# Kernel optimization log

Hardware: AMD Instinct MI355X
Metric: run time of the kernel (lower is better)

## Reference

```python
import jax, jax.numpy as jnp
import numpy as np


def _segment_mean(msg, dst, num_nodes):
    # msg: [E, B, O, T] summed into [N, B, O, T], mean over incoming edges
    s = jax.ops.segment_sum(msg, dst, num_segments=num_nodes)
    cnt = jax.ops.segment_sum(jnp.ones((msg.shape[0],), msg.dtype), dst, num_segments=num_nodes)
    return s / jnp.clip(cnt, 1.0)[:, None, None, None]


def _gcn(x, edge_index, edge_attr, A, Wk, Wr, b):
    # Edge-conditioned (spline-style) graph conv.
    # x: [B, N, Cin, T]; edge_attr: [E, 3]; Wk: [K, Cin, Cout]
    N = x.shape[1]
    src, dst = edge_index[0], edge_index[1]
    Bw = jax.nn.softmax(edge_attr @ A, axis=-1)          # [E, K] basis weights
    We = jnp.einsum('ek,kio->eio', Bw, Wk)                # [E, Cin, Cout]
    msg = jnp.einsum('beit,eio->ebot', x[:, src], We)     # [E, B, Cout, T]
    agg = _segment_mean(msg, dst, N).transpose(1, 0, 2, 3)  # [B, N, Cout, T]
    out = agg + jnp.einsum('bnit,io->bnot', x, Wr) + b[None, None, :, None]
    return jax.nn.elu(out)


def _pool(x, P, C, T):
    # x: [B, N_l, C, T] -> flatten, sparse-pool with P [N_{l+1}, N_l], unflatten
    B, N = x.shape[0], x.shape[1]
    xf = x.reshape(B, N, C * T)
    xf = jnp.einsum('mn,bnf->bmf', P, xf)
    return xf.reshape(B, P.shape[0], C, T)


def setup_inputs() -> dict:
    key = jax.random.key(0)
    ks = jax.random.split(key, 24)
    B, T = 2, 200
    N = [2048, 512, 128, 64]
    E = [16384, 8192, 2048]
    nf = [1, 8, 16, 32, 64, 128, 128]
    ld = 64

    def rn(k, shape, scale=1.0):
        return jax.random.normal(k, shape, dtype=jnp.float32) * scale

    inp = {}
    inp['x'] = rn(ks[0], (B, N[0], nf[0], T))
    inp['ei0'] = jax.random.randint(ks[1], (2, E[0]), 0, N[0])
    inp['ea0'] = jax.random.uniform(ks[2], (E[0], 3), dtype=jnp.float32)
    inp['ei1'] = jax.random.randint(ks[3], (2, E[1]), 0, N[1])
    inp['ea1'] = jax.random.uniform(ks[4], (E[1], 3), dtype=jnp.float32)
    inp['ei2'] = jax.random.randint(ks[5], (2, E[2]), 0, N[2])
    inp['ea2'] = jax.random.uniform(ks[6], (E[2], 3), dtype=jnp.float32)
    # gcn params: (A basis map, K=3 kernel weights, root weight, bias)
    inp['A1'] = rn(ks[7], (3, 3))
    inp['Wk1'] = rn(ks[8], (3, nf[0], nf[2]), 1.0 / np.sqrt(nf[0]))
    inp['Wr1'] = rn(ks[9], (nf[0], nf[2]), 1.0 / np.sqrt(nf[0]))
    inp['b1'] = jnp.zeros((nf[2],), jnp.float32)
    inp['A2'] = rn(ks[10], (3, 3))
    inp['Wk2'] = rn(ks[11], (3, nf[2], nf[3]), 1.0 / np.sqrt(nf[2]))
    inp['Wr2'] = rn(ks[12], (nf[2], nf[3]), 1.0 / np.sqrt(nf[2]))
    inp['b2'] = jnp.zeros((nf[3],), jnp.float32)
    inp['A3'] = rn(ks[13], (3, 3))
    inp['Wk3'] = rn(ks[14], (3, nf[3], nf[4]), 1.0 / np.sqrt(nf[3]))
    inp['Wr3'] = rn(ks[15], (nf[3], nf[4]), 1.0 / np.sqrt(nf[3]))
    inp['b3'] = jnp.zeros((nf[4],), jnp.float32)
    # sparse pooling projections (dense here)
    inp['P01'] = rn(ks[16], (N[1], N[0]), 1.0 / np.sqrt(N[0]))
    inp['P12'] = rn(ks[17], (N[2], N[1]), 1.0 / np.sqrt(N[1]))
    inp['P23'] = rn(ks[18], (N[3], N[2]), 1.0 / np.sqrt(N[2]))
    # 1x1 conv encoder head
    inp['fce1_w'] = rn(ks[19], (nf[4], nf[6]), 1.0 / np.sqrt(nf[4]))
    inp['fce1_b'] = jnp.zeros((nf[6],), jnp.float32)
    inp['fce2_w'] = rn(ks[20], (nf[6], ld), 1.0 / np.sqrt(nf[6]))
    inp['fce2_b'] = jnp.zeros((ld,), jnp.float32)
    return inp


def reference(x, ei0, ea0, ei1, ea1, ei2, ea2, A1, Wk1, Wr1, b1, A2, Wk2, Wr2, b2,
              A3, Wk3, Wr3, b3, P01, P12, P23, fce1_w, fce1_b, fce2_w, fce2_b):
    T = x.shape[-1]
    # level 0 -> 1
    h = _gcn(x, ei0, ea0, A1, Wk1, Wr1, b1)          # [B, N0, 16, T]
    h = _pool(h, P01, h.shape[2], T)                 # [B, N1, 16, T]
    # level 1 -> 2
    h = _gcn(h, ei1, ea1, A2, Wk2, Wr2, b2)          # [B, N1, 32, T]
    h = _pool(h, P12, h.shape[2], T)                 # [B, N2, 32, T]
    # level 2 -> 3
    h = _gcn(h, ei2, ea2, A3, Wk3, Wr3, b3)          # [B, N2, 64, T]
    h = _pool(h, P23, h.shape[2], T)                 # [B, N3, 64, T]
    # 1x1 conv encoder head (channel-wise linear over node/time grid)
    h = jax.nn.elu(jnp.einsum('bnct,co->bnot', h, fce1_w) + fce1_b[None, None, :, None])
    mu = jnp.tanh(jnp.einsum('bnct,co->bnot', h, fce2_w) + fce2_b[None, None, :, None])
    return mu  # [B, N3, latent_dim, T]
```

## Files before the change

kernel.cpp:

```cpp
#include <hip/hip_runtime.h>
#include <hip/hip_bf16.h>

using bf16 = __hip_bfloat16;
typedef unsigned short ushort_t;
typedef unsigned int uint_t;

constexpr int B = 2, T = 200;
constexpr int N0 = 2048, N1 = 512, N2 = 128, N3 = 64;
constexpr int E0 = 16384, E1 = 8192, E2 = 2048;

typedef __attribute__((ext_vector_type(8))) short bf16x8;
typedef __attribute__((ext_vector_type(4))) float f32x4;

constexpr size_t O_FLAG = 161792;
constexpr size_t O_WC1  = 163840;
constexpr size_t O_BIAS = 164096;
constexpr size_t O_BW0  = 165312;
constexpr size_t O_BW1  = 361920;
constexpr size_t O_BW2  = 460224;
constexpr size_t O_PB1  = 484800;
constexpr size_t O_PB2  = 2581952;
constexpr size_t O_PB3  = 2713024;
constexpr size_t O_WT2  = 2729408;
constexpr size_t O_WT3  = 2733504;
constexpr size_t O_W1H  = 2749888;
constexpr size_t O_W2H  = 2766272;
constexpr size_t O_AA   = 2785280;
constexpr size_t O_BB   = 15892480;

__device__ __forceinline__ float ldx(const void* p, long i, int bf) {
  if (bf) {
    uint_t v = (uint_t)(((const ushort_t*)p)[i]) << 16;
    float f; __builtin_memcpy(&f, &v, 4); return f;
  }
  return ((const float*)p)[i];
}
__device__ __forceinline__ void stf(float* p, float v) { *p = v; }
__device__ __forceinline__ void stf(bf16* p, float v) { *p = __float2bfloat16(v); }
__device__ __forceinline__ ushort_t f2bfu(float v) {
  bf16 h = __float2bfloat16(v); ushort_t u; __builtin_memcpy(&u, &h, 2); return u;
}

struct InPtrs {
  const void* ea0; const void* ea1; const void* ea2;
  const void* P01; const void* P12; const void* P23;
  const void* Wk1; const void* Wr1; const void* Wk2; const void* Wr2;
  const void* Wk3; const void* Wr3; const void* W1h; const void* W2h;
  const void* b1; const void* b2; const void* b3; const void* b1h; const void* b2h;
  const void* A1; const void* A2; const void* A3;
};

__global__ void k_setup0(int* I, const ushort_t* ea) {
  if (blockIdx.x < 158) {
    int i = blockIdx.x * 256 + threadIdx.x;
    I[i] = 0;
  } else if (threadIdx.x == 0) {
    int c = 0;
    for (int i = 0; i < 128; ++i) {
      uint_t v = (uint_t)ea[i] << 16;
      float f; __builtin_memcpy(&f, &v, 4);
      if (f >= 0.f && f <= 1.0f) c++;
    }
    *(int*)((char*)I + O_FLAG) = (c >= 120) ? 1 : 0;
  }
}

__device__ __forceinline__ void bw_one(const void* ea, int bf, const void* A,
                                       float* bw, int e) {
  float a0 = ldx(ea, e*3+0, bf), a1 = ldx(ea, e*3+1, bf), a2 = ldx(ea, e*3+2, bf);
  float l0 = a0*ldx(A,0,bf) + a1*ldx(A,3,bf) + a2*ldx(A,6,bf);
  float l1 = a0*ldx(A,1,bf) + a1*ldx(A,4,bf) + a2*ldx(A,7,bf);
  float l2 = a0*ldx(A,2,bf) + a1*ldx(A,5,bf) + a2*ldx(A,8,bf);
  float m = fmaxf(l0, fmaxf(l1, l2));
  float x0 = expf(l0 - m), x1 = expf(l1 - m), x2 = expf(l2 - m);
  float inv = 1.0f / (x0 + x1 + x2);
  bw[e*3+0] = x0*inv; bw[e*3+1] = x1*inv; bw[e*3+2] = x2*inv;
}

__global__ void k_prep(InPtrs P, char* base) {
  int bf = *(const int*)(base + O_FLAG);
  int bx = blockIdx.x, tid = threadIdx.x;
  float* bw0 = (float*)(base + O_BW0);
  float* bw1 = (float*)(base + O_BW1);
  float* bw2 = (float*)(base + O_BW2);
  if (bx < 64)        { bw_one(P.ea0, bf, P.A1, bw0, bx*256+tid); return; }
  if (bx < 96)        { bw_one(P.ea1, bf, P.A2, bw1, (bx-64)*256+tid); return; }
  if (bx < 104)       { bw_one(P.ea2, bf, P.A3, bw2, (bx-96)*256+tid); return; }
  if (bx < 4200)      { long i = (long)(bx-104)*256+tid;
                        ((ushort_t*)(base+O_PB1))[i] = f2bfu(ldx(P.P01, i, bf)); return; }
  if (bx < 4456)      { int i = (bx-4200)*256+tid;
                        ((ushort_t*)(base+O_PB2))[i] = f2bfu(ldx(P.P12, i, bf)); return; }
  if (bx < 4488)      { int i = (bx-4456)*256+tid;
                        ((ushort_t*)(base+O_PB3))[i] = f2bfu(ldx(P.P23, i, bf)); return; }
  if (bx < 4496)      { int j = (bx-4488)*256+tid; int o = j>>6, c = j&63;
                        float v = (c<48) ? ldx(P.Wk2, c*32+o, bf) : ldx(P.Wr2, (c-48)*32+o, bf);
                        ((ushort_t*)(base+O_WT2))[j] = f2bfu(v); return; }
  if (bx < 4528)      { int j = (bx-4496)*256+tid; int o = j>>7, c = j&127;
                        float v = (c<96) ? ldx(P.Wk3, c*64+o, bf) : ldx(P.Wr3, (c-96)*64+o, bf);
                        ((ushort_t*)(base+O_WT3))[j] = f2bfu(v); return; }
  if (bx < 4560)      { int j = (bx-4528)*256+tid; int o = j>>6, c = j&63;
                        ((ushort_t*)(base+O_W1H))[j] = f2bfu(ldx(P.W1h, c*128+o, bf)); return; }
  if (bx < 4592)      { int j = (bx-4560)*256+tid; int o = j>>7, c = j&127;
                        ((ushort_t*)(base+O_W2H))[j] = f2bfu(ldx(P.W2h, c*64+o, bf)); return; }
  {
    int i = (bx-4592)*256+tid;
    if (i < 64) {
      ((float*)(base+O_WC1))[i] = (i<48) ? ldx(P.Wk1, i, bf) : ldx(P.Wr1, i-48, bf);
    } else if (i < 368) {
      int j = i - 64; float v;
      if (j < 16)       v = ldx(P.b1, j, bf);
      else if (j < 48)  v = ldx(P.b2, j-16, bf);
      else if (j < 112) v = ldx(P.b3, j-48, bf);
      else if (j < 240) v = ldx(P.b1h, j-112, bf);
      else              v = ldx(P.b2h, j-240, bf);
      ((float*)(base+O_BIAS))[j] = v;
    }
  }
}

__global__ void k_hist3(const int* d0, const int* d1, const int* d2,
                        int* c0, int* c1, int* c2) {
  int i = blockIdx.x * 256 + threadIdx.x;
  if (i < E0) atomicAdd(&c0[d0[i]], 1);
  if (i < E1) atomicAdd(&c1[d1[i]], 1);
  if (i < E2) atomicAdd(&c2[d2[i]], 1);
}

__global__ void k_scan3(const int* c0, int* o0, int* u0,
                        const int* c1, int* o1, int* u1,
                        const int* c2, int* o2, int* u2) {
  const int* cnt; int* off; int* cur; int N;
  if (blockIdx.x == 0)      { cnt = c0; off = o0; cur = u0; N = N0; }
  else if (blockIdx.x == 1) { cnt = c1; off = o1; cur = u1; N = N1; }
  else                      { cnt = c2; off = o2; cur = u2; N = N2; }
  int tid = threadIdx.x;
  int chunk = (N + 63) >> 6;
  int base = tid * chunk;
  int s = 0;
  for (int j = 0; j < chunk; ++j) { int idx = base + j; if (idx < N) s += cnt[idx]; }
  int pre = s;
  for (int d = 1; d < 64; d <<= 1) {
    int v = __shfl_up(pre, d, 64);
    if (tid >= d) pre += v;
  }
  int run = pre - s;
  for (int j = 0; j < chunk; ++j) {
    int idx = base + j;
    if (idx < N) { off[idx] = run; cur[idx] = run; run += cnt[idx]; }
  }
  if (tid == 63) off[N] = run;
}

__global__ void k_fill3(const int* d0, int* u0, int* e0l,
                        const int* d1, int* u1, int* e1l,
                        const int* d2, int* u2, int* e2l) {
  int i = blockIdx.x * 256 + threadIdx.x;
  if (i < E0) { int p = atomicAdd(&u0[d0[i]], 1); e0l[p] = i; }
  if (i < E1) { int p = atomicAdd(&u1[d1[i]], 1); e1l[p] = i; }
  if (i < E2) { int p = atomicAdd(&u2[d2[i]], 1); e2l[p] = i; }
}

__global__ __launch_bounds__(256) void k_gc1(const void* x, const int* src,
    const int* off, const int* elist, const int* cnt, const float* bw,
    const float* W, const float* bias, bf16* h1, const int* flagp) {
  __shared__ float Wl[64];
  __shared__ float bl[16];
  __shared__ float ew0[32], ew1[32], ew2[32];
  __shared__ int es[32];
  int tid = threadIdx.x;
  if (tid < 64) Wl[tid] = W[tid];
  if (tid < 16) bl[tid] = bias[tid];
  int bf = *flagp;
  int n = blockIdx.y, b = blockIdx.z;
  int t = tid;
  bool tok = t < T;
  int beg = off[n], end = off[n + 1];
  float a0 = 0.f, a1 = 0.f, a2 = 0.f;
  for (int q0 = beg; q0 < end; q0 += 32) {
    int m = end - q0; if (m > 32) m = 32;
    __syncthreads();
    if (tid < m) {
      int e = elist[q0 + tid];
      es[tid] = src[e];
      ew0[tid] = bw[e*3+0]; ew1[tid] = bw[e*3+1]; ew2[tid] = bw[e*3+2];
    }
    __syncthreads();
    if (tok) {
      for (int j = 0; j < m; ++j) {
        float xv = ldx(x, (long)(b * N0 + es[j]) * T + t, bf);
        a0 += ew0[j] * xv; a1 += ew1[j] * xv; a2 += ew2[j] * xv;
      }
    }
  }
  __syncthreads();
  if (!tok) return;
  int c = cnt[n];
  float inv = 1.f / (float)(c > 0 ? c : 1);
  a0 *= inv; a1 *= inv; a2 *= inv;
  float xr = ldx(x, (long)(b * N0 + n) * T + t, bf);
  bf16* op = h1 + ((long)(b * N0 + n) * 16) * T + t;
#pragma unroll
  for (int o = 0; o < 16; ++o) {
    float v = a0 * Wl[o] + a1 * Wl[16 + o] + a2 * Wl[32 + o] + xr * Wl[48 + o] + bl[o];
    v = v > 0.f ? v : (expf(v) - 1.f);
    op[o * T] = __float2bfloat16(v);
  }
}

template<int CIN, int CPI, int O>
__global__ __launch_bounds__(256) void k_gcm(const float* hp, const int* src,
    const int* off, const int* elist, const int* cnt, const float* bw,
    const ushort_t* Wt, const float* bias, bf16* h, int N) {
  constexpr int C = 4 * CIN;
  constexpr int KG = C / 8;
  constexpr int MT = O / 16;
  __shared__ __align__(16) ushort_t Ws[O * C];
  __shared__ __align__(16) ushort_t Is[64 * C];
  __shared__ float ew0[32], ew1[32], ew2[32];
  __shared__ int es[32];
  int tid = threadIdx.x;
  int w = tid >> 6, l = tid & 63;
  int lf = l & 15, quad = l >> 4;
  int t0 = blockIdx.x * 64;
  int n = blockIdx.y, b = blockIdx.z;
  {
    const uint4* Wg = (const uint4*)Wt;
    for (int s = tid; s < O * KG; s += 256) {
      int o = s / KG, kg = s % KG;
      *(uint4*)(Ws + o * C + ((kg ^ (o & 7)) * 8)) = Wg[s];
    }
  }
  int tx = tid & 63, iy = tid >> 6;
  int t = t0 + tx;
  bool tok = t < T;
  float acc[3][CPI], xr[CPI];
#pragma unroll
  for (int k = 0; k < 3; ++k)
#pragma unroll
    for (int j = 0; j < CPI; ++j) acc[k][j] = 0.f;
#pragma unroll
  for (int j = 0; j < CPI; ++j) xr[j] = 0.f;
  int beg = off[n], end = off[n + 1];
  for (int q0 = beg; q0 < end; q0 += 32) {
    int mE = end - q0; if (mE > 32) mE = 32;
    __syncthreads();
    if (tid < mE) {
      int e = elist[q0 + tid];
      es[tid] = src[e];
      ew0[tid] = bw[e*3+0]; ew1[tid] = bw[e*3+1]; ew2[tid] = bw[e*3+2];
    }
    __syncthreads();
    if (tok) {
      for (int j2 = 0; j2 < mE; ++j2) {
        int s = es[j2];
        float w0 = ew0[j2], w1 = ew1[j2], w2 = ew2[j2];
        const float* xp = hp + ((long)(b * N + s) * CIN) * T + t;
#pragma unroll
        for (int j = 0; j < CPI; ++j) {
          float xv = xp[(iy * CPI + j) * T];
          acc[0][j] += w0 * xv; acc[1][j] += w1 * xv; acc[2][j] += w2 * xv;
        }
      }
    }
  }
  float inv = 1.f;
  if (tok) {
    int c = cnt[n];
    inv = 1.f / (float)(c > 0 ? c : 1);
    const float* xs = hp + ((long)(b * N + n) * CIN) * T + t;
#pragma unroll
    for (int j = 0; j < CPI; ++j) xr[j] = xs[(iy * CPI + j) * T];
  }
#pragma unroll
  for (int j = 0; j < CPI; ++j) {
    int i = iy * CPI + j;
#pragma unroll
    for (int k = 0; k < 3; ++k) {
      int c = k * CIN + i;
      Is[tx * C + ((c >> 3) ^ (tx & 7)) * 8 + (c & 7)] = f2bfu(acc[k][j] * inv);
    }
    int c = 3 * CIN + i;
    Is[tx * C + ((c >> 3) ^ (tx & 7)) * 8 + (c & 7)] = f2bfu(xr[j]);
  }
  __syncthreads();
  f32x4 dacc[MT];
#pragma unroll
  for (int mt = 0; mt < MT; ++mt) dacc[mt] = (f32x4){0.f, 0.f, 0.f, 0.f};
  int tr = w * 16 + lf;
#pragma unroll
  for (int kc = 0; kc < C / 32; ++kc) {
    int kg0 = kc * 4 + quad;
    bf16x8 bfr = *(const bf16x8*)(Is + tr * C + ((kg0 ^ (tr & 7)) * 8));
#pragma unroll
    for (int mt = 0; mt < MT; ++mt) {
      int o = mt * 16 + lf;
      bf16x8 afr = *(const bf16x8*)(Ws + o * C + ((kg0 ^ (o & 7)) * 8));
      dacc[mt] = __builtin_amdgcn_mfma_f32_16x16x32_bf16(afr, bfr, dacc[mt], 0, 0, 0);
    }
  }
  int tg = t0 + w * 16 + lf;
  if (tg < T) {
    long nb = (long)(b * N + n) * O;
#pragma unroll
    for (int mt = 0; mt < MT; ++mt) {
#pragma unroll
      for (int r = 0; r < 4; ++r) {
        int o = mt * 16 + quad * 4 + r;
        float v = dacc[mt][r] + bias[o];
        v = v > 0.f ? v : (expf(v) - 1.f);
        h[(nb + o) * T + tg] = __float2bfloat16(v);
      }
    }
  }
}

template<int KSPLIT, bool ATOMIC, bool SWZ>
__global__ __launch_bounds__(256) void k_poolp(const ushort_t* Pb, const ushort_t* h,
                                               float* out, int M, int K, int F, int nInner) {
  __shared__ __align__(16) ushort_t As[64 * 64];
  __shared__ __align__(16) ushort_t Bs[64 * 64];
  int tid = threadIdx.x;
  int w = tid >> 6, l = tid & 63;
  int lf = l & 15, quad = l >> 4;
  int v = blockIdx.x;
  if (SWZ) { int q = gridDim.x >> 3; v = (v & 7) * q + (v >> 3); }
  int f_blk = v / nInner; int rem = v % nInner;
  int m_blk = rem / (KSPLIT * B);
  int kc = (rem / B) % KSPLIT;
  int b = rem % B;
  int f0 = f_blk * 64, m0 = m_blk * 64;
  int Kc = K / KSPLIT;
  int k0 = kc * Kc;
  int nsteps = Kc >> 6;

  int am0 = tid >> 3, ak = tid & 7;
  int am1 = am0 + 32;
  const ushort_t* Ap0 = Pb + (long)(m0 + am0) * K + k0 + ak * 8;
  const ushort_t* Ap1 = Pb + (long)(m0 + am1) * K + k0 + ak * 8;
  int fB = tid & 63, kb = (tid >> 6) * 16;
  const ushort_t* Bp = h + ((long)b * K + k0 + kb) * F + f0 + fB;
  int kc0 = kb >> 3;

#define PLA(r0, r1, st) { r0 = *(const uint4*)(Ap0 + (st) * 64); \
                          r1 = *(const uint4*)(Ap1 + (st) * 64); }
#define PLB(rb, st) { _Pragma("unroll") \
                      for (int i = 0; i < 16; ++i) rb[i] = Bp[(long)((st) * 64 + i) * F]; }
#define PSA(r0, r1) { *(uint4*)(As + am0 * 64 + ((ak ^ (am0 & 7)) * 8)) = r0; \
                      *(uint4*)(As + am1 * 64 + ((ak ^ (am1 & 7)) * 8)) = r1; }
#define PSB(rb) { *(uint4*)(Bs + fB * 64 + ((kc0 ^ (fB & 7)) * 8)) = *(uint4*)&rb[0]; \
                  *(uint4*)(Bs + fB * 64 + (((kc0 + 1) ^ (fB & 7)) * 8)) = *(uint4*)&rb[8]; }
#define PMM() { _Pragma("unroll") for (int ks = 0; ks < 2; ++ks) { \
    int kq = ks * 4 + quad; \
    bf16x8 bfr[4]; \
    _Pragma("unroll") for (int ft = 0; ft < 4; ++ft) { int fl = ft * 16 + lf; \
      bfr[ft] = *(const bf16x8*)(Bs + fl * 64 + ((kq ^ (fl & 7)) * 8)); } \
    int ml = w * 16 + lf; \
    bf16x8 afr = *(const bf16x8*)(As + ml * 64 + ((kq ^ (ml & 7)) * 8)); \
    _Pragma("unroll") for (int ft = 0; ft < 4; ++ft) \
      acc[ft] = __builtin_amdgcn_mfma_f32_16x16x32_bf16(afr, bfr[ft], acc[ft], 0, 0, 0); } }

  f32x4 acc[4];
#pragma unroll
  for (int ft = 0; ft < 4; ++ft) acc[ft] = (f32x4){0.f, 0.f, 0.f, 0.f};

  uint4 ra0, ra1, sa0, sa1;
  ushort_t rb[16], sb[16];
  PLA(ra0, ra1, 0); PLB(rb, 0);
  for (int s = 0; s < nsteps; s += 2) {
    PLA(sa0, sa1, s + 1); PLB(sb, s + 1);
    __syncthreads();
    PSA(ra0, ra1); PSB(rb);
    __syncthreads();
    PMM();
    if (s + 2 < nsteps) { PLA(ra0, ra1, s + 2); PLB(rb, s + 2); }
    __syncthreads();
    PSA(sa0, sa1); PSB(sb);
    __syncthreads();
    PMM();
  }
#undef PLA
#undef PLB
#undef PSA
#undef PSB
#undef PMM

#pragma unroll
  for (int r = 0; r < 4; ++r) {
    int m = m0 + w * 16 + quad * 4 + r;
    float* op = out + ((long)(b * M + m)) * F + f0 + lf;
#pragma unroll
    for (int ft = 0; ft < 4; ++ft) {
      if (ATOMIC) atomicAdd(op + ft * 16, acc[ft][r]);
      else        op[ft * 16] = acc[ft][r];
    }
  }
}

__global__ __launch_bounds__(256) void k_head(const float* hp3, const ushort_t* W1t,
    const ushort_t* W2t, const float* bias, void* outp, const int* flagp) {
  __shared__ __align__(16) ushort_t Ws1[128 * 64];
  __shared__ __align__(16) ushort_t Ws2[64 * 128];
  __shared__ __align__(16) ushort_t Is[64 * 64];
  __shared__ __align__(16) ushort_t G[64 * 128];
  int tid = threadIdx.x;
  int w = tid >> 6, l = tid & 63;
  int lf = l & 15, quad = l >> 4;
  int t0 = blockIdx.x * 64;
  int n = blockIdx.y, b = blockIdx.z;
  {
    const uint4* g1 = (const uint4*)W1t;
    for (int s = tid; s < 1024; s += 256) {
      int o = s >> 3, kg = s & 7;
      *(uint4*)(Ws1 + o * 64 + ((kg ^ (o & 7)) * 8)) = g1[s];
    }
    const uint4* g2 = (const uint4*)W2t;
    for (int s = tid; s < 1024; s += 256) {
      int o = s >> 4, kg = s & 15;
      *(uint4*)(Ws2 + o * 128 + ((kg ^ (o & 7)) * 8)) = g2[s];
    }
  }
  {
    int t = tid & 63;
    bool tok = (t0 + t) < T;
    const float* ip = hp3 + ((long)(b * 64 + n) * 64) * T + t0;
    for (int kg = tid >> 6; kg < 8; kg += 4) {
      ushort_t r[8];
#pragma unroll
      for (int j = 0; j < 8; ++j)
        r[j] = tok ? f2bfu(ip[(kg * 8 + j) * T + t]) : (ushort_t)0;
      *(uint4*)(Is + t * 64 + ((kg ^ (t & 7)) * 8)) = *(uint4*)r;
    }
  }
  __syncthreads();
  int tr = w * 16 + lf;
  {
    f32x4 a1[8];
#pragma unroll
    for (int mt = 0; mt < 8; ++mt) a1[mt] = (f32x4){0.f, 0.f, 0.f, 0.f};
#pragma unroll
    for (int kc = 0; kc < 2; ++kc) {
      int kg0 = kc * 4 + quad;
      bf16x8 bfr = *(const bf16x8*)(Is + tr * 64 + ((kg0 ^ (tr & 7)) * 8));
#pragma unroll
      for (int mt = 0; mt < 8; ++mt) {
        int o = mt * 16 + lf;
        bf16x8 afr = *(const bf16x8*)(Ws1 + o * 64 + ((kg0 ^ (o & 7)) * 8));
        a1[mt] = __builtin_amdgcn_mfma_f32_16x16x32_bf16(afr, bfr, a1[mt], 0, 0, 0);
      }
    }
    int tG = w * 16 + lf;
#pragma unroll
    for (int mt = 0; mt < 8; ++mt) {
#pragma unroll
      for (int r = 0; r < 4; ++r) {
        int o1 = mt * 16 + quad * 4 + r;
        float v = a1[mt][r] + bias[112 + o1];
        v = v > 0.f ? v : (expf(v) - 1.f);
        G[tG * 128 + ((o1 >> 3) ^ (tG & 7)) * 8 + (o1 & 7)] = f2bfu(v);
      }
    }
  }
  __syncthreads();
  {
    f32x4 a2[4];
#pragma unroll
    for (int mt = 0; mt < 4; ++mt) a2[mt] = (f32x4){0.f, 0.f, 0.f, 0.f};
#pragma unroll
    for (int kc = 0; kc < 4; ++kc) {
      int kg0 = kc * 4 + quad;
      bf16x8 bfr = *(const bf16x8*)(G + tr * 128 + ((kg0 ^ (tr & 7)) * 8));
#pragma unroll
      for (int mt = 0; mt < 4; ++mt) {
        int o = mt * 16 + lf;
        bf16x8 afr = *(const bf16x8*)(Ws2 + o * 128 + ((kg0 ^ (o & 7)) * 8));
        a2[mt] = __builtin_amdgcn_mfma_f32_16x16x32_bf16(afr, bfr, a2[mt], 0, 0, 0);
      }
    }
    int t = t0 + w * 16 + lf;
    if (t < T) {
      int bf = *flagp;
      long nb = (long)(b * 64 + n) * 64;
#pragma unroll
      for (int mt = 0; mt < 4; ++mt) {
#pragma unroll
        for (int r = 0; r < 4; ++r) {
          int o2 = mt * 16 + quad * 4 + r;
          float v = tanhf(a2[mt][r] + bias[240 + o2]);
          long idx = (nb + o2) * T + t;
          if (bf) ((bf16*)outp)[idx] = __float2bfloat16(v);
          else    ((float*)outp)[idx] = v;
        }
      }
    }
  }
}

extern "C" void kernel_launch(void* const* d_in, const int* in_sizes, int n_in,
                              void* d_out, int out_size, void* d_ws, size_t ws_size,
                              hipStream_t stream) {
  const int* ei0 = (const int*)d_in[1];
  const int* ei1 = (const int*)d_in[3];
  const int* ei2 = (const int*)d_in[5];

  char* base = (char*)d_ws;
  int* I = (int*)base;
  int* cnt0 = I;         int* off0 = I + 2048;  int* cur0 = I + 4112;  int* el0 = I + 6160;
  int* cnt1 = I + 22544; int* off1 = I + 23056; int* cur1 = I + 23584; int* el1 = I + 24096;
  int* cnt2 = I + 32288; int* off2 = I + 32416; int* cur2 = I + 32560; int* el2 = I + 32688;
  const int* flagp = (const int*)(base + O_FLAG);
  float* wc1f = (float*)(base + O_WC1);
  float* bias = (float*)(base + O_BIAS);
  float* bw0 = (float*)(base + O_BW0);
  float* bw1 = (float*)(base + O_BW1);
  float* bw2 = (float*)(base + O_BW2);
  ushort_t* Pb1 = (ushort_t*)(base + O_PB1);
  ushort_t* Pb2 = (ushort_t*)(base + O_PB2);
  ushort_t* Pb3 = (ushort_t*)(base + O_PB3);
  ushort_t* wt2 = (ushort_t*)(base + O_WT2);
  ushort_t* wt3 = (ushort_t*)(base + O_WT3);
  ushort_t* w1t = (ushort_t*)(base + O_W1H);
  ushort_t* w2t = (ushort_t*)(base + O_W2H);
  char* Aa = base + O_AA;
  char* Bb = base + O_BB;

  InPtrs P = { d_in[2], d_in[4], d_in[6], d_in[19], d_in[20], d_in[21],
               d_in[8], d_in[9], d_in[12], d_in[13], d_in[16], d_in[17],
               d_in[22], d_in[24], d_in[10], d_in[14], d_in[18], d_in[23],
               d_in[25], d_in[7], d_in[11], d_in[15] };

  k_setup0<<<159, 256, 0, stream>>>(I, (const ushort_t*)d_in[2]);
  k_prep<<<4594, 256, 0, stream>>>(P, base);
  k_hist3<<<64, 256, 0, stream>>>(ei0 + E0, ei1 + E1, ei2 + E2, cnt0, cnt1, cnt2);
  k_scan3<<<3, 64, 0, stream>>>(cnt0, off0, cur0, cnt1, off1, cur1, cnt2, off2, cur2);
  k_fill3<<<64, 256, 0, stream>>>(ei0 + E0, cur0, el0, ei1 + E1, cur1, el1, ei2 + E2, cur2, el2);

  hipMemsetAsync(Aa, 0, (size_t)13107200, stream);
  k_gc1<<<dim3(1, N0, B), 256, 0, stream>>>(d_in[0], ei0, off0, el0, cnt0, bw0, wc1f, bias, (bf16*)Bb, flagp);
  k_poolp<2, true, true><<<1600, 256, 0, stream>>>(Pb1, (const ushort_t*)Bb, (float*)Aa, 512, 2048, 3200, 32);
  k_gcm<16, 4, 32><<<dim3(4, N1, B), 256, 0, stream>>>((const float*)Aa, ei1, off1, el1, cnt1, bw1, wt2, bias + 16, (bf16*)Bb, N1);
  hipMemsetAsync(Aa, 0, (size_t)6553600, stream);
  k_poolp<2, true, true><<<800, 256, 0, stream>>>(Pb2, (const ushort_t*)Bb, (float*)Aa, 128, 512, 6400, 8);
  k_gcm<32, 8, 64><<<dim3(4, N2, B), 256, 0, stream>>>((const float*)Aa, ei2, off2, el2, cnt2, bw2, wt3, bias + 48, (bf16*)Bb, N2);
  k_poolp<1, false, false><<<400, 256, 0, stream>>>(Pb3, (const ushort_t*)Bb, (float*)Aa, 64, 128, 12800, 2);
  k_head<<<dim3(4, N3, B), 256, 0, stream>>>((const float*)Aa, w1t, w2t, bias, d_out, flagp);
}
```

Before: 302.4 us.

## Double-buffer pool GEMM LDS tiles and drop split-K atomics with memsets

Rewrites the pooling GEMM kernel to use two LDS buffers per operand, so the MFMA work on one tile overlaps the shared-memory stores of the next. This halves the barriers per step and replaces __syncthreads with a lighter waitcnt plus barrier. It also removes the split-K decomposition, along with its float atomics and the two memsets that zeroed the output. In exchange each block does twice the K work and the grid has half as many blocks, which lowers parallelism on the large pooling stages.

```diff
diff --git a/kernel.cpp b/kernel.cpp
--- a/kernel.cpp
+++ b/kernel.cpp
@@ -314,85 +314,86 @@
   }
 }
 
-template<int KSPLIT, bool ATOMIC, bool SWZ>
+template<bool SWZ>
 __global__ __launch_bounds__(256) void k_poolp(const ushort_t* Pb, const ushort_t* h,
                                                float* out, int M, int K, int F, int nInner) {
-  __shared__ __align__(16) ushort_t As[64 * 64];
-  __shared__ __align__(16) ushort_t Bs[64 * 64];
+  __shared__ __align__(16) ushort_t As0[64 * 64];
+  __shared__ __align__(16) ushort_t As1[64 * 64];
+  __shared__ __align__(16) ushort_t Bs0[64 * 64];
+  __shared__ __align__(16) ushort_t Bs1[64 * 64];
   int tid = threadIdx.x;
   int w = tid >> 6, l = tid & 63;
   int lf = l & 15, quad = l >> 4;
   int v = blockIdx.x;
   if (SWZ) { int q = gridDim.x >> 3; v = (v & 7) * q + (v >> 3); }
   int f_blk = v / nInner; int rem = v % nInner;
-  int m_blk = rem / (KSPLIT * B);
-  int kc = (rem / B) % KSPLIT;
-  int b = rem % B;
+  int m_blk = rem >> 1;
+  int b = rem & 1;
   int f0 = f_blk * 64, m0 = m_blk * 64;
-  int Kc = K / KSPLIT;
-  int k0 = kc * Kc;
-  int nsteps = Kc >> 6;
+  int nsteps = K >> 6;
 
   int am0 = tid >> 3, ak = tid & 7;
   int am1 = am0 + 32;
-  const ushort_t* Ap0 = Pb + (long)(m0 + am0) * K + k0 + ak * 8;
-  const ushort_t* Ap1 = Pb + (long)(m0 + am1) * K + k0 + ak * 8;
+  const ushort_t* Ap0 = Pb + (long)(m0 + am0) * K + ak * 8;
+  const ushort_t* Ap1 = Pb + (long)(m0 + am1) * K + ak * 8;
   int fB = tid & 63, kb = (tid >> 6) * 16;
-  const ushort_t* Bp = h + ((long)b * K + k0 + kb) * F + f0 + fB;
+  const ushort_t* Bp = h + ((long)b * K + kb) * F + f0 + fB;
   int kc0 = kb >> 3;
 
-#define PLA(r0, r1, st) { r0 = *(const uint4*)(Ap0 + (st) * 64); \
-                          r1 = *(const uint4*)(Ap1 + (st) * 64); }
+#define PLA(r0, r1, st) { r0 = *(const uint4*)(Ap0 + (long)(st) * 64); \
+                          r1 = *(const uint4*)(Ap1 + (long)(st) * 64); }
 #define PLB(rb, st) { _Pragma("unroll") \
-                      for (int i = 0; i < 16; ++i) rb[i] = Bp[(long)((st) * 64 + i) * F]; }
-#define PSA(r0, r1) { *(uint4*)(As + am0 * 64 + ((ak ^ (am0 & 7)) * 8)) = r0; \
-                      *(uint4*)(As + am1 * 64 + ((ak ^ (am1 & 7)) * 8)) = r1; }
-#define PSB(rb) { *(uint4*)(Bs + fB * 64 + ((kc0 ^ (fB & 7)) * 8)) = *(uint4*)&rb[0]; \
-                  *(uint4*)(Bs + fB * 64 + (((kc0 + 1) ^ (fB & 7)) * 8)) = *(uint4*)&rb[8]; }
-#define PMM() { _Pragma("unroll") for (int ks = 0; ks < 2; ++ks) { \
+                      for (int i = 0; i < 16; ++i) rb[i] = Bp[((long)(st) * 64 + i) * F]; }
+#define PSA(S, r0, r1) { *(uint4*)(S + am0 * 64 + ((ak ^ (am0 & 7)) * 8)) = r0; \
+                         *(uint4*)(S + am1 * 64 + ((ak ^ (am1 & 7)) * 8)) = r1; }
+#define PSB(S, rb) { *(uint4*)(S + fB * 64 + ((kc0 ^ (fB & 7)) * 8)) = *(uint4*)&rb[0]; \
+                     *(uint4*)(S + fB * 64 + (((kc0 + 1) ^ (fB & 7)) * 8)) = *(uint4*)&rb[8]; }
+#define PMM(SA, SB) { _Pragma("unroll") for (int ks = 0; ks < 2; ++ks) { \
     int kq = ks * 4 + quad; \
     bf16x8 bfr[4]; \
     _Pragma("unroll") for (int ft = 0; ft < 4; ++ft) { int fl = ft * 16 + lf; \
-      bfr[ft] = *(const bf16x8*)(Bs + fl * 64 + ((kq ^ (fl & 7)) * 8)); } \
+      bfr[ft] = *(const bf16x8*)(SB + fl * 64 + ((kq ^ (fl & 7)) * 8)); } \
     int ml = w * 16 + lf; \
-    bf16x8 afr = *(const bf16x8*)(As + ml * 64 + ((kq ^ (ml & 7)) * 8)); \
+    bf16x8 afr = *(const bf16x8*)(SA + ml * 64 + ((kq ^ (ml & 7)) * 8)); \
     _Pragma("unroll") for (int ft = 0; ft < 4; ++ft) \
       acc[ft] = __builtin_amdgcn_mfma_f32_16x16x32_bf16(afr, bfr[ft], acc[ft], 0, 0, 0); } }
+#define BARW() { asm volatile("s_waitcnt lgkmcnt(0)" ::: "memory"); \
+                 __builtin_amdgcn_s_barrier(); \
+                 asm volatile("" ::: "memory"); }
 
   f32x4 acc[4];
 #pragma unroll
   for (int ft = 0; ft < 4; ++ft) acc[ft] = (f32x4){0.f, 0.f, 0.f, 0.f};
 
-  uint4 ra0, ra1, sa0, sa1;
-  ushort_t rb[16], sb[16];
-  PLA(ra0, ra1, 0); PLB(rb, 0);
-  for (int s = 0; s < nsteps; s += 2) {
-    PLA(sa0, sa1, s + 1); PLB(sb, s + 1);
-    __syncthreads();
-    PSA(ra0, ra1); PSB(rb);
-    __syncthreads();
-    PMM();
-    if (s + 2 < nsteps) { PLA(ra0, ra1, s + 2); PLB(rb, s + 2); }
-    __syncthreads();
-    PSA(sa0, sa1); PSB(sb);
-    __syncthreads();
-    PMM();
+  uint4 xa0, xa1, ya0, ya1;
+  ushort_t xb[16], yb[16];
+  PLA(xa0, xa1, 0); PLB(xb, 0);
+  PLA(ya0, ya1, 1); PLB(yb, 1);
+  PSA(As0, xa0, xa1); PSB(Bs0, xb);
+  BARW();
+  for (int e = 0; e < nsteps; e += 2) {
+    if (e + 2 < nsteps) { PLA(xa0, xa1, e + 2); PLB(xb, e + 2); }
+    PMM(As0, Bs0);
+    PSA(As1, ya0, ya1); PSB(Bs1, yb);
+    BARW();
+    if (e + 3 < nsteps) { PLA(ya0, ya1, e + 3); PLB(yb, e + 3); }
+    PMM(As1, Bs1);
+    if (e + 2 < nsteps) { PSA(As0, xa0, xa1); PSB(Bs0, xb); }
+    BARW();
   }
 #undef PLA
 #undef PLB
 #undef PSA
 #undef PSB
 #undef PMM
+#undef BARW
 
 #pragma unroll
   for (int r = 0; r < 4; ++r) {
     int m = m0 + w * 16 + quad * 4 + r;
     float* op = out + ((long)(b * M + m)) * F + f0 + lf;
 #pragma unroll
-    for (int ft = 0; ft < 4; ++ft) {
-      if (ATOMIC) atomicAdd(op + ft * 16, acc[ft][r]);
-      else        op[ft * 16] = acc[ft][r];
-    }
+    for (int ft = 0; ft < 4; ++ft) op[ft * 16] = acc[ft][r];
   }
 }
 
@@ -534,13 +535,11 @@
   k_scan3<<<3, 64, 0, stream>>>(cnt0, off0, cur0, cnt1, off1, cur1, cnt2, off2, cur2);
   k_fill3<<<64, 256, 0, stream>>>(ei0 + E0, cur0, el0, ei1 + E1, cur1, el1, ei2 + E2, cur2, el2);
 
-  hipMemsetAsync(Aa, 0, (size_t)13107200, stream);
   k_gc1<<<dim3(1, N0, B), 256, 0, stream>>>(d_in[0], ei0, off0, el0, cnt0, bw0, wc1f, bias, (bf16*)Bb, flagp);
-  k_poolp<2, true, true><<<1600, 256, 0, stream>>>(Pb1, (const ushort_t*)Bb, (float*)Aa, 512, 2048, 3200, 32);
+  k_poolp<true><<<800, 256, 0, stream>>>(Pb1, (const ushort_t*)Bb, (float*)Aa, 512, 2048, 3200, 16);
   k_gcm<16, 4, 32><<<dim3(4, N1, B), 256, 0, stream>>>((const float*)Aa, ei1, off1, el1, cnt1, bw1, wt2, bias + 16, (bf16*)Bb, N1);
-  hipMemsetAsync(Aa, 0, (size_t)6553600, stream);
-  k_poolp<2, true, true><<<800, 256, 0, stream>>>(Pb2, (const ushort_t*)Bb, (float*)Aa, 128, 512, 6400, 8);
+  k_poolp<true><<<400, 256, 0, stream>>>(Pb2, (const ushort_t*)Bb, (float*)Aa, 128, 512, 6400, 4);
   k_gcm<32, 8, 64><<<dim3(4, N2, B), 256, 0, stream>>>((const float*)Aa, ei2, off2, el2, cnt2, bw2, wt3, bias + 48, (bf16*)Bb, N2);
-  k_poolp<1, false, false><<<400, 256, 0, stream>>>(Pb3, (const ushort_t*)Bb, (float*)Aa, 64, 128, 12800, 2);
+  k_poolp<false><<<400, 256, 0, stream>>>(Pb3, (const ushort_t*)Bb, (float*)Aa, 64, 128, 12800, 2);
   k_head<<<dim3(4, N3, B), 256, 0, stream>>>((const float*)Aa, w1t, w2t, bias, d_out, flagp);
 }
```

Result: faster. 283.7 us (-6.2%).
